# Optimization experiments

Measured on AMD Instinct MI355X. Metric: run time of the kernel, lower is better.

Reference implementation:

```python
import jax, jax.numpy as jnp
import numpy as np

# dims (see shape_source)
B, N, P, H, M, E, HOPS = 512, 102, 12, 256, 4, 3, 2
C_CLIP = 10.0   # logit clipping constant params['C']
T = 1.0         # temperature params['T']
NEG = -1e9


def setup_inputs() -> dict:
    key = jax.random.key(0)
    ks = jax.random.split(key, 18)
    s = 0.08  # uniform init range as in _initialize_weights, use scaled normals
    inp = {
        "node_features": jax.random.normal(ks[0], (B, N, P), jnp.float32),
        "adjacency": jax.random.uniform(ks[1], (B, E, N, N), jnp.float32),  # per-edge-cat weighted adjacency
        "mask": jax.random.randint(ks[2], (B, N), 0, 2).astype(jnp.int32),  # 1 = already scheduled / forbidden
        # encoder params
        "W_emb": jax.random.normal(ks[3], (P, H), jnp.float32) * s,
        "W_rel": jax.random.normal(ks[4], (HOPS, E, H, H), jnp.float32) * s / np.sqrt(H),
        "W_self": jax.random.normal(ks[5], (HOPS, H, H), jnp.float32) * s / np.sqrt(H),
        # multi-head glimpse params (Vec / W_q / W_ref per head)
        "Vec": jax.random.normal(ks[6], (M, H, H), jnp.float32) * s,
        "W_q": jax.random.normal(ks[7], (M, 3 * H, H), jnp.float32) * s,
        "W_ref": jax.random.normal(ks[8], (M, H, H), jnp.float32) * s,
        "W_mh": jax.random.normal(ks[9], (M * H, H), jnp.float32) * s,  # multi_head_embedding
        # final pointer params
        "Vec2": jax.random.normal(ks[10], (H,), jnp.float32) * s,
        "W_q2": jax.random.normal(ks[11], (H, H), jnp.float32) * s,
        "W_ref2": jax.random.normal(ks[12], (H, H), jnp.float32) * s,
        # learned decoder seed vectors
        "dec_input": jax.random.normal(ks[13], (H,), jnp.float32) * s,
        "v_1": jax.random.normal(ks[14], (H,), jnp.float32) * s,
    }
    return inp


def reference(node_features, adjacency, mask, W_emb, W_rel, W_self, Vec, W_q,
              W_ref, W_mh, Vec2, W_q2, W_ref2, dec_input, v_1):
    # ---- encoder: linear embedding + HOPS of relational (per-edge-category) message passing ----
    h = jnp.einsum('bnp,ph->bnh', node_features, W_emb)            # [B,N,H]
    for hop in range(HOPS):
        msg = jnp.einsum('benm,bmh->benh', adjacency, h)           # gather neighbors per edge cat
        h = jax.nn.relu(jnp.einsum('benh,ehk->bnk', msg, W_rel[hop])
                        + jnp.einsum('bnh,hk->bnk', h, W_self[hop]))
    enc = h                                                         # [B,N,H]

    # ---- decoder query: cat(graph readout, learned dec_input, learned v_1) -> 3H ----
    enc_mean = enc.mean(axis=1)                                     # [B,H]
    q_cat = jnp.concatenate([enc_mean,
                             jnp.broadcast_to(dec_input, (B, H)),
                             jnp.broadcast_to(v_1, (B, H))], axis=-1)  # [B,3H]

    # ---- multi-head additive (Bahdanau) glimpse: per-head Vec/W_q/W_ref tanh scoring ----
    q = jnp.einsum('bf,mfh->bmh', q_cat, W_q)                       # [B,M,H]
    r = jnp.einsum('bnh,mhk->bmnk', enc, W_ref)                     # [B,M,N,H]
    u = jnp.einsum('bmnh,mhk->bmnk', jnp.tanh(q[:, :, None, :] + r), Vec)
    scores = u.sum(axis=-1)                                         # [B,M,N]
    scores = jnp.where(mask[:, None, :] > 0, NEG, scores)
    a = jax.nn.softmax(scores, axis=-1)
    ctx = jnp.einsum('bmn,bnh->bmh', a, enc).reshape(B, M * H)
    query2 = ctx @ W_mh                                             # [B,H]

    # ---- final pointer head (Vec2 / W_q2 / W_ref2) ----
    u2 = jnp.einsum('h,bnh->bn', Vec2,
                    jnp.tanh((query2 @ W_q2)[:, None, :] + jnp.einsum('bnh,hk->bnk', enc, W_ref2)))
    u2 = C_CLIP * jnp.tanh(u2)                                      # logit clipping
    u2 = jnp.where(mask > 0, NEG, u2)
    log_p = jax.nn.log_softmax(u2 / T, axis=-1)                     # [B,N]
    return log_p
```

## Files before the change

### kernel.cpp

```cpp
#include <hip/hip_runtime.h>
#include <hip/hip_bf16.h>

#define B 512
#define N 102
#define Pdim 12
#define H 256
#define M 4
#define E 3
#define NEG (-1e9f)
#define RT 52224
#define NN 10404

typedef __hip_bfloat16 bf16;
typedef __attribute__((ext_vector_type(8))) short short8;
typedef __attribute__((ext_vector_type(4))) float f32x4;
typedef __attribute__((ext_vector_type(16))) float f32x16;

__device__ __forceinline__ float b2f(bf16 v) { return __bfloat162float(v); }
__device__ __forceinline__ bf16 f2b(float v) { return __float2bfloat16(v); }
__device__ __forceinline__ short f2bs(float v) {
    bf16 t = __float2bfloat16(v);
    return *reinterpret_cast<short*>(&t);
}
__device__ __forceinline__ float fast_tanh(float x) {
    float e = __expf(2.f * x);
    return 1.f - 2.f * __builtin_amdgcn_rcpf(e + 1.f);
}

__global__ __launch_bounds__(256) void wt_prep(const float* __restrict__ Wrel,
                                               const float* __restrict__ Wself,
                                               const float* __restrict__ Wref,
                                               const float* __restrict__ Wref2,
                                               const float* __restrict__ Wmh,
                                               const float* __restrict__ Wq2,
                                               const float* __restrict__ W_q,
                                               const float* __restrict__ Vec,
                                               const float* __restrict__ W_emb,
                                               const float* __restrict__ dec,
                                               const float* __restrict__ v1,
                                               const float* __restrict__ adj,
                                               short* __restrict__ wfrag,
                                               short* __restrict__ wrefT,
                                               short* __restrict__ wref2T,
                                               short* __restrict__ wmh_bf,
                                               short* __restrict__ wq2_bf,
                                               short* __restrict__ wq_bf,
                                               short* __restrict__ wembf,
                                               short* __restrict__ adjp,
                                               float* __restrict__ qconst,
                                               float* __restrict__ vsum) {
    int bid = blockIdx.x;
    int tid = threadIdx.x;
    __shared__ short tl[1024 * 17];
    if (bid >= 3652) {
        int be = bid - 3652;
        const float* src = adj + (size_t)be * NN;
        short* dst = adjp + (size_t)be * (112 * 128);
        for (int i = tid; i < 112 * 128; i += 256) {
            int n = i >> 7, m = i & 127;
            short v = 0;
            if (n < N && m < N) v = f2bs(src[n * N + m]);
            dst[i] = v;
        }
        return;
    }
    if (bid < 32) {
        int hop = bid >> 4, ct = bid & 15;
        for (int i = tid; i < 16384; i += 256) {
            int k = i >> 4, c0 = i & 15;
            int c = ct * 16 + c0;
            float v;
            if (k < 768) v = Wrel[(((size_t)hop * E + (k >> 8)) * H + (k & 255)) * H + c];
            else         v = Wself[((size_t)hop * H + (k - 768)) * H + c];
            tl[k * 17 + c0] = f2bs(v);
        }
        __syncthreads();
        short8* outp = (short8*)wfrag + (size_t)(hop * 16 + ct) * 2048;
        for (int i = tid; i < 2048; i += 256) {
            int ks = i >> 6, lq = i & 63;
            int c0 = lq & 15, kb = (lq >> 4) * 8;
            short8 v;
#pragma unroll
            for (int j = 0; j < 8; ++j) v[j] = tl[(ks * 32 + kb + j) * 17 + c0];
            outp[i] = v;
        }
        return;
    }
    if (bid >= 3648) {
        int m = bid - 3648, hh = tid;
        __shared__ float dls[H], vls[H];
        dls[hh] = dec[hh];
        vls[hh] = v1[hh];
        __syncthreads();
        const float* Wm = W_q + (size_t)m * (3 * H) * H;
        float s = 0.f;
        for (int f = 0; f < H; ++f)
            s += dls[f] * Wm[(H + f) * H + hh] + vls[f] * Wm[(2 * H + f) * H + hh];
        qconst[m * H + hh] = s;
        float vs = 0.f;
        const float* Vr = Vec + ((size_t)m * H + hh) * H;
        for (int k = 0; k < H; ++k) vs += Vr[k];
        vsum[m * H + hh] = vs;
        return;
    }
    int idx = 524288 + (bid - 32) * 256 + tid;
    if (idx < 786432) {
        int r = idx - 524288;
        int row = r >> 8, k = r & 255;
        int m = row >> 8, c = row & 255;
        wrefT[r] = f2bs(Wref[((size_t)m * H + k) * H + c]);
    } else if (idx < 851968) {
        int r = idx - 786432;
        int c = r >> 8, k = r & 255;
        wref2T[r] = f2bs(Wref2[k * H + c]);
    } else if (idx < 1114112) {
        int r = idx - 851968;
        wmh_bf[r] = f2bs(Wmh[r]);
    } else if (idx < 1179648) {
        int r = idx - 1114112;
        wq2_bf[r] = f2bs(Wq2[r]);
    } else if (idx < 1441792) {
        int r = idx - 1179648;
        int m = r >> 16, fh = r & 65535;
        wq_bf[r] = f2bs(W_q[(size_t)m * 768 * 256 + fh]);
    } else if (idx < 1449984) {
        int r = idx - 1441792;
        int ct = r >> 9, lq = (r >> 3) & 63, j = r & 7;
        int c = ct * 16 + (lq & 15), k = (lq >> 4) * 8 + j;
        wembf[r] = (k < Pdim) ? f2bs(W_emb[k * H + c]) : (short)0;
    }
}

#define HP 264
#define YP2 136
#define ASP 136
__global__ __launch_bounds__(512, 2) void enc_fused(const float* __restrict__ nf,
                                                    const short* __restrict__ wembf,
                                                    const short* __restrict__ adjp,
                                                    const short* __restrict__ wfragp,
                                                    bf16* __restrict__ enc_out,
                                                    float* __restrict__ mean_out) {
    int b = blockIdx.x;
    int tid = threadIdx.x;
    int w = tid >> 6;
    int l = tid & 63;
    int cg = l & 15;
    int rg = l >> 4;
    int ct0 = 2 * w, ct1 = ct0 + 1;

    __shared__ short hS[112 * HP];
    __shared__ short YtS[256 * YP2];
    __shared__ short AsS[112 * ASP];

    const short8 z8 = {0, 0, 0, 0, 0, 0, 0, 0};
    for (int i = tid; i < 10 * 32; i += 512) {
        int n = 102 + (i >> 5), g = i & 31;
        *(short8*)(&hS[n * HP + g * 8]) = z8;
    }
    {
        int c = tid >> 1, g = 14 + (tid & 1);
        *(short8*)(&YtS[c * YP2 + g * 8]) = z8;
    }

    {
        const short8* we8 = (const short8*)wembf;
        short8 bfe0 = we8[ct0 * 64 + l];
        short8 bfe1 = we8[ct1 * 64 + l];
#pragma unroll
        for (int nt = 0; nt < 7; ++nt) {
            int row = nt * 16 + cg;
            short8 afr = z8;
            if (row < 102 && rg < 2) {
                const float* src = nf + ((size_t)b * N + row) * Pdim + rg * 8;
                f32x4 v0 = *(const f32x4*)src;
                afr[0] = f2bs(v0[0]); afr[1] = f2bs(v0[1]);
                afr[2] = f2bs(v0[2]); afr[3] = f2bs(v0[3]);
                if (rg == 0) {
                    f32x4 v1 = *(const f32x4*)(src + 4);
                    afr[4] = f2bs(v1[0]); afr[5] = f2bs(v1[1]);
                    afr[6] = f2bs(v1[2]); afr[7] = f2bs(v1[3]);
                }
            }
            f32x4 d0 = (f32x4){0.f, 0.f, 0.f, 0.f}, d1 = d0;
            d0 = __builtin_amdgcn_mfma_f32_16x16x32_bf16(afr, bfe0, d0, 0, 0, 0);
            d1 = __builtin_amdgcn_mfma_f32_16x16x32_bf16(afr, bfe1, d1, 0, 0, 0);
#pragma unroll
            for (int r = 0; r < 4; ++r) {
                int n = nt * 16 + rg * 4 + r;
                hS[n * HP + ct0 * 16 + cg] = f2bs(d0[r]);
                hS[n * HP + ct1 * 16 + cg] = f2bs(d1[r]);
            }
        }
    }
    __syncthreads();

    for (int hop = 0; hop < 2; ++hop) {
        const short8* wf8 = ((const short8*)wfragp) + (size_t)hop * 32768;
        f32x4 hacc0[7], hacc1[7];
#pragma unroll
        for (int j = 0; j < 7; ++j) {
            hacc0[j] = (f32x4){0.f, 0.f, 0.f, 0.f};
            hacc1[j] = hacc0[j];
        }

        for (int e = 0; e < E; ++e) {
            const short8* Ap = (const short8*)adjp + (size_t)(b * E + e) * 1792;
            for (int i = tid; i < 1792; i += 512) {
                int n = i >> 4, g = i & 15;
                *(short8*)(&AsS[n * ASP + g * 8]) = Ap[i];
            }
            if (e == 0) {
#pragma unroll
                for (int ks = 0; ks < 8; ++ks) {
                    short8 wfs0 = wf8[(ct0 * 32 + 24 + ks) * 64 + l];
                    short8 wfs1 = wf8[(ct1 * 32 + 24 + ks) * 64 + l];
#pragma unroll
                    for (int nt = 0; nt < 7; ++nt) {
                        short8 hf = *(const short8*)(&hS[(nt * 16 + cg) * HP + ks * 32 + rg * 8]);
                        hacc0[nt] = __builtin_amdgcn_mfma_f32_16x16x32_bf16(hf, wfs0, hacc0[nt], 0, 0, 0);
                        hacc1[nt] = __builtin_amdgcn_mfma_f32_16x16x32_bf16(hf, wfs1, hacc1[nt], 0, 0, 0);
                    }
                }
            }
            f32x4 g0[7], g1[7];
#pragma unroll
            for (int j = 0; j < 7; ++j) {
                g0[j] = (f32x4){0.f, 0.f, 0.f, 0.f};
                g1[j] = g0[j];
            }
#pragma unroll
            for (int ks = 0; ks < 8; ++ks) {
                short8 wfa0 = wf8[(ct0 * 32 + e * 8 + ks) * 64 + l];
                short8 wfa1 = wf8[(ct1 * 32 + e * 8 + ks) * 64 + l];
#pragma unroll
                for (int mt = 0; mt < 7; ++mt) {
                    short8 hf = *(const short8*)(&hS[(mt * 16 + cg) * HP + ks * 32 + rg * 8]);
                    g0[mt] = __builtin_amdgcn_mfma_f32_16x16x32_bf16(wfa0, hf, g0[mt], 0, 0, 0);
                    g1[mt] = __builtin_amdgcn_mfma_f32_16x16x32_bf16(wfa1, hf, g1[mt], 0, 0, 0);
                }
            }
#pragma unroll
            for (int mt = 0; mt < 7; ++mt)
#pragma unroll
                for (int r = 0; r < 4; ++r) {
                    int c0 = ct0 * 16 + rg * 4 + r;
                    int c1 = ct1 * 16 + rg * 4 + r;
                    YtS[c0 * YP2 + mt * 16 + cg] = f2bs(g0[mt][r]);
                    YtS[c1 * YP2 + mt * 16 + cg] = f2bs(g1[mt][r]);
                }
            __syncthreads();
#pragma unroll
            for (int ks = 0; ks < 4; ++ks) {
                short8 yf0 = *(const short8*)(&YtS[(ct0 * 16 + cg) * YP2 + (ks * 4 + rg) * 8]);
                short8 yf1 = *(const short8*)(&YtS[(ct1 * 16 + cg) * YP2 + (ks * 4 + rg) * 8]);
#pragma unroll
                for (int nt = 0; nt < 7; ++nt) {
                    short8 af = *(const short8*)(&AsS[(nt * 16 + cg) * ASP + ks * 32 + rg * 8]);
                    hacc0[nt] = __builtin_amdgcn_mfma_f32_16x16x32_bf16(af, yf0, hacc0[nt], 0, 0, 0);
                    hacc1[nt] = __builtin_amdgcn_mfma_f32_16x16x32_bf16(af, yf1, hacc1[nt], 0, 0, 0);
                }
            }
            __syncthreads();
        }
#pragma unroll
        for (int nt = 0; nt < 7; ++nt)
#pragma unroll
            for (int r = 0; r < 4; ++r) {
                int n = nt * 16 + rg * 4 + r;
                float v0 = hacc0[nt][r], v1 = hacc1[nt][r];
                hS[n * HP + ct0 * 16 + cg] = f2bs(v0 > 0.f ? v0 : 0.f);
                hS[n * HP + ct1 * 16 + cg] = f2bs(v1 > 0.f ? v1 : 0.f);
            }
        __syncthreads();
    }

    short* ho = (short*)enc_out;
    for (int i = tid; i < 102 * 32; i += 512) {
        int n = i >> 5, g = i & 31;
        *(short8*)(ho + ((size_t)b * N + n) * H + g * 8) = *(const short8*)(&hS[n * HP + g * 8]);
    }
    {
        float* partf = (float*)AsS;
        int c = tid & 255, qq = tid >> 8;
        float s = 0.f;
        for (int n = qq; n < N; n += 2) s += b2f(*(const bf16*)&hS[n * HP + c]);
        partf[qq * 256 + c] = s;
        __syncthreads();
        if (tid < 256)
            mean_out[(size_t)b * H + tid] = (partf[tid] + partf[256 + tid]) * (1.f / (float)N);
    }
}

__global__ __launch_bounds__(256, 2) void head2_mfma(const bf16* __restrict__ X,
                                                     const short* __restrict__ WT,
                                                     const float* __restrict__ qb, int qbs,
                                                     const float* __restrict__ vsb,
                                                     float* __restrict__ outp, int obs) {
    int rt = blockIdx.x, m = blockIdx.y;
    int r0 = rt * 128;
    int tid = threadIdx.x;
    int w = tid >> 6, l = tid & 63;
    int lr = l & 31;
    int lh = l >> 5;
    __shared__ short Xs[128 * 256];
    __shared__ float qls[3 * 256];
    __shared__ float part[4][128];

    const short* Xp = (const short*)X;
#pragma unroll
    for (int i = 0; i < 16; ++i) {
        int id = tid + i * 256;
        int r = id >> 5, g = id & 31;
        short8 v = *(const short8*)(Xp + (size_t)(r0 + r) * H + g * 8);
        *(short8*)((char*)Xs + r * 512 + ((g ^ (r & 7)) * 16)) = v;
    }
    int b_base = r0 / N;
#pragma unroll
    for (int i = 0; i < 3; ++i) {
        int bb = b_base + i;
        if (bb > B - 1) bb = B - 1;
        qls[i * 256 + tid] = qb[(size_t)bb * qbs + m * H + tid];
    }
    const short8* w8 = (const short8*)WT;
    int cbase = m * 256 + w * 64;
    short8 afr0[16], afr1[16];
#pragma unroll
    for (int ks = 0; ks < 16; ++ks) {
        afr0[ks] = w8[(size_t)(cbase + lr) * 32 + ks * 2 + lh];
        afr1[ks] = w8[(size_t)(cbase + 32 + lr) * 32 + ks * 2 + lh];
    }
    float vsl[32];
#pragma unroll
    for (int j = 0; j < 16; ++j) {
        int cl = (j & 3) + 8 * (j >> 2) + 4 * lh;
        vsl[j]      = vsb[m * H + w * 64 + cl];
        vsl[16 + j] = vsb[m * H + w * 64 + 32 + cl];
    }
    __syncthreads();

    int swz = lr & 7;
    for (int t = 0; t < 4; ++t) {
        f32x16 acc0, acc1;
#pragma unroll
        for (int j = 0; j < 16; ++j) { acc0[j] = 0.f; acc1[j] = 0.f; }
        const char* xbase = (const char*)Xs + (t * 32 + lr) * 512;
#pragma unroll
        for (int ks = 0; ks < 16; ++ks) {
            short8 bx = *(const short8*)(xbase + (((2 * ks + lh) ^ swz) * 16));
            acc0 = __builtin_amdgcn_mfma_f32_32x32x16_bf16(afr0[ks], bx, acc0, 0, 0, 0);
            acc1 = __builtin_amdgcn_mfma_f32_32x32x16_bf16(afr1[ks], bx, acc1, 0, 0, 0);
        }
        int r = r0 + t * 32 + lr;
        int b = r / N;
        int boff = b - b_base;
        float s = 0.f;
#pragma unroll
        for (int j = 0; j < 16; ++j) {
            int cl = (j & 3) + 8 * (j >> 2) + 4 * lh;
            float x0 = qls[boff * 256 + w * 64 + cl] + acc0[j];
            s += fast_tanh(x0) * vsl[j];
            float x1 = qls[boff * 256 + w * 64 + 32 + cl] + acc1[j];
            s += fast_tanh(x1) * vsl[16 + j];
        }
        s += __shfl_xor(s, 32, 64);
        if (l < 32) part[w][t * 32 + lr] = s;
    }
    __syncthreads();
    if (tid < 128) {
        int r = r0 + tid;
        int b = r / N, n = r - b * N;
        outp[(size_t)b * obs + m * N + n] = part[0][tid] + part[1][tid] + part[2][tid] + part[3][tid];
    }
}

__global__ __launch_bounds__(256) void q_k(const float* __restrict__ enc_mean,
                                           const short* __restrict__ wq_bf,
                                           const float* __restrict__ qconst,
                                           float* __restrict__ qbuf) {
    int bid = blockIdx.x;
    int b = bid >> 2, m = bid & 3;
    int hh = threadIdx.x;
    __shared__ float em[H];
    em[hh] = enc_mean[(size_t)b * H + hh];
    __syncthreads();
    const bf16* Wm = (const bf16*)(wq_bf + (size_t)m * 65536);
    float s = qconst[m * H + hh];
    for (int f = 0; f < H; ++f) s += em[f] * b2f(Wm[f * H + hh]);
    qbuf[((size_t)b * M + m) * H + hh] = s;
}

__global__ __launch_bounds__(256) void softmax_ctx_k(const float* __restrict__ scores,
                                                     const int* __restrict__ mask,
                                                     const bf16* __restrict__ enc,
                                                     float* __restrict__ ctx) {
    int bid = blockIdx.x;
    int b = bid >> 2, m = bid & 3;
    int tid = threadIdx.x;
    __shared__ float a[128];
    __shared__ float red[2];
    float sv = NEG;
    if (tid < N)
        sv = (mask[(size_t)b * N + tid] > 0) ? NEG : scores[((size_t)b * M + m) * N + tid];
    if (tid < 128) a[tid] = sv;
    __syncthreads();
    if (tid < 64) {
        float v = fmaxf(a[tid], a[tid + 64]);
        v = fmaxf(v, __shfl_xor(v, 32, 64));
        v = fmaxf(v, __shfl_xor(v, 16, 64));
        v = fmaxf(v, __shfl_xor(v, 8, 64));
        v = fmaxf(v, __shfl_xor(v, 4, 64));
        v = fmaxf(v, __shfl_xor(v, 2, 64));
        v = fmaxf(v, __shfl_xor(v, 1, 64));
        if (tid == 0) red[0] = v;
    }
    __syncthreads();
    float mx = red[0];
    float ev = (tid < N) ? __expf(sv - mx) : 0.f;
    if (tid < 128) a[tid] = ev;
    __syncthreads();
    if (tid < 64) {
        float v = a[tid] + a[tid + 64];
        v += __shfl_xor(v, 32, 64);
        v += __shfl_xor(v, 16, 64);
        v += __shfl_xor(v, 8, 64);
        v += __shfl_xor(v, 4, 64);
        v += __shfl_xor(v, 2, 64);
        v += __shfl_xor(v, 1, 64);
        if (tid == 0) red[1] = __builtin_amdgcn_rcpf(v);
    }
    __syncthreads();
    float inv = red[1];
    float c = 0.f;
    for (int n = 0; n < N; ++n)
        c += a[n] * b2f(enc[((size_t)b * N + n) * H + tid]);
    ctx[((size_t)b * M + m) * H + tid] = c * inv;
}

__global__ __launch_bounds__(256) void query2_k(const float* __restrict__ ctx,
                                                const short* __restrict__ wmh,
                                                const short* __restrict__ wq2,
                                                float* __restrict__ q2) {
    int b = blockIdx.x;
    int tid = threadIdx.x;
    __shared__ float cx[M * H];
    __shared__ float qy[H];
    for (int idx = tid; idx < M * H; idx += 256) cx[idx] = ctx[(size_t)b * M * H + idx];
    __syncthreads();
    const bf16* wm = (const bf16*)wmh;
    float acc = 0.f;
    for (int j = 0; j < M * H; ++j) acc += cx[j] * b2f(wm[(size_t)j * H + tid]);
    qy[tid] = acc;
    __syncthreads();
    const bf16* w2 = (const bf16*)wq2;
    float acc2 = 0.f;
    for (int k = 0; k < H; ++k) acc2 += qy[k] * b2f(w2[(size_t)k * H + tid]);
    q2[(size_t)b * H + tid] = acc2;
}

__global__ __launch_bounds__(128) void final_out_k(const float* __restrict__ u2,
                                                   const int* __restrict__ mask,
                                                   float* __restrict__ out) {
    int b = blockIdx.x;
    int tid = threadIdx.x;
    __shared__ float a[128];
    __shared__ float red[2];
    float u = NEG;
    if (tid < N) {
        u = 10.f * fast_tanh(u2[(size_t)b * N + tid]);
        if (mask[(size_t)b * N + tid] > 0) u = NEG;
    }
    a[tid] = u;
    __syncthreads();
    if (tid < 64) {
        float v = fmaxf(a[tid], a[tid + 64]);
        v = fmaxf(v, __shfl_xor(v, 32, 64));
        v = fmaxf(v, __shfl_xor(v, 16, 64));
        v = fmaxf(v, __shfl_xor(v, 8, 64));
        v = fmaxf(v, __shfl_xor(v, 4, 64));
        v = fmaxf(v, __shfl_xor(v, 2, 64));
        v = fmaxf(v, __shfl_xor(v, 1, 64));
        if (tid == 0) red[0] = v;
    }
    __syncthreads();
    float mx = red[0];
    float ev = (tid < N) ? __expf(u - mx) : 0.f;
    a[tid] = ev;
    __syncthreads();
    if (tid < 64) {
        float v = a[tid] + a[tid + 64];
        v += __shfl_xor(v, 32, 64);
        v += __shfl_xor(v, 16, 64);
        v += __shfl_xor(v, 8, 64);
        v += __shfl_xor(v, 4, 64);
        v += __shfl_xor(v, 2, 64);
        v += __shfl_xor(v, 1, 64);
        if (tid == 0) red[1] = logf(v);
    }
    __syncthreads();
    if (tid < N) out[(size_t)b * N + tid] = (u - mx) - red[1];
}

extern "C" void kernel_launch(void* const* d_in, const int* in_sizes, int n_in,
                              void* d_out, int out_size, void* d_ws, size_t ws_size,
                              hipStream_t stream) {
    const float* nf     = (const float*)d_in[0];
    const float* adj    = (const float*)d_in[1];
    const int*   mask   = (const int*)d_in[2];
    const float* W_emb  = (const float*)d_in[3];
    const float* W_rel  = (const float*)d_in[4];
    const float* W_self = (const float*)d_in[5];
    const float* Vec    = (const float*)d_in[6];
    const float* W_q    = (const float*)d_in[7];
    const float* W_ref  = (const float*)d_in[8];
    const float* W_mh   = (const float*)d_in[9];
    const float* Vec2   = (const float*)d_in[10];
    const float* W_q2   = (const float*)d_in[11];
    const float* W_ref2 = (const float*)d_in[12];
    const float* dec    = (const float*)d_in[13];
    const float* v_1    = (const float*)d_in[14];
    float* out = (float*)d_out;

    char* p = (char*)d_ws;
    size_t off = 0;
    auto alloc = [&](size_t bytes) -> char* {
        char* q = p + off;
        off += (bytes + 255) & ~(size_t)255;
        return q;
    };
    bf16* hA      = (bf16*)alloc((size_t)RT * H * sizeof(bf16));
    short* adjp   = (short*)alloc((size_t)B * E * 112 * 128 * sizeof(short));
    short* wfrag  = (short*)alloc(524288 * sizeof(short));
    short* wrefT  = (short*)alloc(262144 * sizeof(short));
    short* wref2T = (short*)alloc(65536 * sizeof(short));
    short* wmh_bf = (short*)alloc(262144 * sizeof(short));
    short* wq2_bf = (short*)alloc(65536 * sizeof(short));
    short* wq_bf  = (short*)alloc(262144 * sizeof(short));
    short* wembf  = (short*)alloc(8192 * sizeof(short));
    float* enc_mean = (float*)alloc((size_t)B * H * sizeof(float));
    float* qconst   = (float*)alloc((size_t)M * H * sizeof(float));
    float* vsumb    = (float*)alloc((size_t)M * H * sizeof(float));
    float* qbuf     = (float*)alloc((size_t)B * M * H * sizeof(float));
    float* scoresb  = (float*)alloc((size_t)B * M * N * sizeof(float));
    float* ctxb     = (float*)alloc((size_t)B * M * H * sizeof(float));
    float* q2b      = (float*)alloc((size_t)B * H * sizeof(float));
    float* u2b      = (float*)alloc((size_t)B * N * sizeof(float));

    wt_prep<<<5188, 256, 0, stream>>>(W_rel, W_self, W_ref, W_ref2, W_mh, W_q2,
                                      W_q, Vec, W_emb, dec, v_1, adj,
                                      wfrag, wrefT, wref2T, wmh_bf, wq2_bf, wq_bf, wembf,
                                      adjp, qconst, vsumb);

    enc_fused<<<B, 512, 0, stream>>>(nf, wembf, adjp, wfrag, hA, enc_mean);

    const bf16* enc = hA;

    q_k<<<B * M, 256, 0, stream>>>(enc_mean, wq_bf, qconst, qbuf);
    head2_mfma<<<dim3(RT / 128, M), 256, 0, stream>>>(enc, wrefT, qbuf, M * H, vsumb, scoresb, M * N);
    softmax_ctx_k<<<B * M, 256, 0, stream>>>(scoresb, mask, enc, ctxb);
    query2_k<<<B, 256, 0, stream>>>(ctxb, wmh_bf, wq2_bf, q2b);
    head2_mfma<<<dim3(RT / 128, 1), 256, 0, stream>>>(enc, wref2T, q2b, H, Vec2, u2b, N);
    final_out_k<<<B, 128, 0, stream>>>(u2b, mask, out);
}
```

Measured before the change: 270.1 us.

## Fuse adjacency conversion into encoder, widen encoder blocks, loop heads inside scoring kernel

The separate pass that converted and padded the adjacency tensor to bf16 is removed. The encoder now reads fp32 adjacency directly and converts it into shared memory, saving a full global write and re-read of the padded copy. The encoder block grows from 512 to 1024 threads, with each half of the waves taking a subset of the row tiles. The multi-head scoring kernel now loops over all heads inside one block, so the enc tile is loaded into shared memory once instead of once per head. The risks are a scalar, uncoalesced fp32 adjacency load with integer division, and fewer blocks for the head kernel.

```diff
diff --git a/kernel.cpp b/kernel.cpp
--- a/kernel.cpp
+++ b/kernel.cpp
@@ -38,7 +38,6 @@
                                                const float* __restrict__ W_emb,
                                                const float* __restrict__ dec,
                                                const float* __restrict__ v1,
-                                               const float* __restrict__ adj,
                                                short* __restrict__ wfrag,
                                                short* __restrict__ wrefT,
                                                short* __restrict__ wref2T,
@@ -46,24 +45,11 @@
                                                short* __restrict__ wq2_bf,
                                                short* __restrict__ wq_bf,
                                                short* __restrict__ wembf,
-                                               short* __restrict__ adjp,
                                                float* __restrict__ qconst,
                                                float* __restrict__ vsum) {
     int bid = blockIdx.x;
     int tid = threadIdx.x;
     __shared__ short tl[1024 * 17];
-    if (bid >= 3652) {
-        int be = bid - 3652;
-        const float* src = adj + (size_t)be * NN;
-        short* dst = adjp + (size_t)be * (112 * 128);
-        for (int i = tid; i < 112 * 128; i += 256) {
-            int n = i >> 7, m = i & 127;
-            short v = 0;
-            if (n < N && m < N) v = f2bs(src[n * N + m]);
-            dst[i] = v;
-        }
-        return;
-    }
     if (bid < 32) {
         int hop = bid >> 4, ct = bid & 15;
         for (int i = tid; i < 16384; i += 256) {
@@ -134,32 +120,43 @@
 #define HP 264
 #define YP2 136
 #define ASP 136
-__global__ __launch_bounds__(512, 2) void enc_fused(const float* __restrict__ nf,
-                                                    const short* __restrict__ wembf,
-                                                    const short* __restrict__ adjp,
-                                                    const short* __restrict__ wfragp,
-                                                    bf16* __restrict__ enc_out,
-                                                    float* __restrict__ mean_out) {
+__global__ __launch_bounds__(1024, 4) void enc_fused(const float* __restrict__ nf,
+                                                     const short* __restrict__ wembf,
+                                                     const float* __restrict__ adj,
+                                                     const short* __restrict__ wfragp,
+                                                     bf16* __restrict__ enc_out,
+                                                     float* __restrict__ mean_out) {
     int b = blockIdx.x;
     int tid = threadIdx.x;
     int w = tid >> 6;
     int l = tid & 63;
     int cg = l & 15;
     int rg = l >> 4;
-    int ct0 = 2 * w, ct1 = ct0 + 1;
+    int cgrp = w & 7;
+    int half = w >> 3;
+    int ct0 = 2 * cgrp, ct1 = ct0 + 1;
+    int t0 = half * 4;
 
     __shared__ short hS[112 * HP];
     __shared__ short YtS[256 * YP2];
     __shared__ short AsS[112 * ASP];
 
     const short8 z8 = {0, 0, 0, 0, 0, 0, 0, 0};
-    for (int i = tid; i < 10 * 32; i += 512) {
+    for (int i = tid; i < 10 * 32; i += 1024) {
         int n = 102 + (i >> 5), g = i & 31;
         *(short8*)(&hS[n * HP + g * 8]) = z8;
     }
-    {
+    if (tid < 512) {
         int c = tid >> 1, g = 14 + (tid & 1);
         *(short8*)(&YtS[c * YP2 + g * 8]) = z8;
+    }
+    for (int i = tid; i < 160; i += 1024) {
+        int n = 102 + (i >> 4), g = i & 15;
+        *(short8*)(&AsS[n * ASP + g * 8]) = z8;
+    }
+    for (int i = tid; i < 102 * 26; i += 1024) {
+        int n = i / 26, m = 102 + (i % 26);
+        AsS[n * ASP + m] = 0;
     }
 
     {
@@ -167,28 +164,31 @@
         short8 bfe0 = we8[ct0 * 64 + l];
         short8 bfe1 = we8[ct1 * 64 + l];
 #pragma unroll
-        for (int nt = 0; nt < 7; ++nt) {
-            int row = nt * 16 + cg;
-            short8 afr = z8;
-            if (row < 102 && rg < 2) {
-                const float* src = nf + ((size_t)b * N + row) * Pdim + rg * 8;
-                f32x4 v0 = *(const f32x4*)src;
-                afr[0] = f2bs(v0[0]); afr[1] = f2bs(v0[1]);
-                afr[2] = f2bs(v0[2]); afr[3] = f2bs(v0[3]);
-                if (rg == 0) {
-                    f32x4 v1 = *(const f32x4*)(src + 4);
-                    afr[4] = f2bs(v1[0]); afr[5] = f2bs(v1[1]);
-                    afr[6] = f2bs(v1[2]); afr[7] = f2bs(v1[3]);
-                }
-            }
-            f32x4 d0 = (f32x4){0.f, 0.f, 0.f, 0.f}, d1 = d0;
-            d0 = __builtin_amdgcn_mfma_f32_16x16x32_bf16(afr, bfe0, d0, 0, 0, 0);
-            d1 = __builtin_amdgcn_mfma_f32_16x16x32_bf16(afr, bfe1, d1, 0, 0, 0);
-#pragma unroll
-            for (int r = 0; r < 4; ++r) {
-                int n = nt * 16 + rg * 4 + r;
-                hS[n * HP + ct0 * 16 + cg] = f2bs(d0[r]);
-                hS[n * HP + ct1 * 16 + cg] = f2bs(d1[r]);
+        for (int j = 0; j < 4; ++j) {
+            if (j < 3 || half == 0) {
+                int nt = t0 + j;
+                int row = nt * 16 + cg;
+                short8 afr = z8;
+                if (row < 102 && rg < 2) {
+                    const float* src = nf + ((size_t)b * N + row) * Pdim + rg * 8;
+                    f32x4 v0 = *(const f32x4*)src;
+                    afr[0] = f2bs(v0[0]); afr[1] = f2bs(v0[1]);
+                    afr[2] = f2bs(v0[2]); afr[3] = f2bs(v0[3]);
+                    if (rg == 0) {
+                        f32x4 v1 = *(const f32x4*)(src + 4);
+                        afr[4] = f2bs(v1[0]); afr[5] = f2bs(v1[1]);
+                        afr[6] = f2bs(v1[2]); afr[7] = f2bs(v1[3]);
+                    }
+                }
+                f32x4 d0 = (f32x4){0.f, 0.f, 0.f, 0.f}, d1 = d0;
+                d0 = __builtin_amdgcn_mfma_f32_16x16x32_bf16(afr, bfe0, d0, 0, 0, 0);
+                d1 = __builtin_amdgcn_mfma_f32_16x16x32_bf16(afr, bfe1, d1, 0, 0, 0);
+#pragma unroll
+                for (int r = 0; r < 4; ++r) {
+                    int n = nt * 16 + rg * 4 + r;
+                    hS[n * HP + ct0 * 16 + cg] = f2bs(d0[r]);
+                    hS[n * HP + ct1 * 16 + cg] = f2bs(d1[r]);
+                }
             }
         }
     }
@@ -196,18 +196,18 @@
 
     for (int hop = 0; hop < 2; ++hop) {
         const short8* wf8 = ((const short8*)wfragp) + (size_t)hop * 32768;
-        f32x4 hacc0[7], hacc1[7];
-#pragma unroll
-        for (int j = 0; j < 7; ++j) {
+        f32x4 hacc0[4], hacc1[4];
+#pragma unroll
+        for (int j = 0; j < 4; ++j) {
             hacc0[j] = (f32x4){0.f, 0.f, 0.f, 0.f};
             hacc1[j] = hacc0[j];
         }
 
         for (int e = 0; e < E; ++e) {
-            const short8* Ap = (const short8*)adjp + (size_t)(b * E + e) * 1792;
-            for (int i = tid; i < 1792; i += 512) {
-                int n = i >> 4, g = i & 15;
-                *(short8*)(&AsS[n * ASP + g * 8]) = Ap[i];
+            const float* Ae = adj + ((size_t)b * E + e) * NN;
+            for (int i = tid; i < NN; i += 1024) {
+                int n = i / N, m = i - n * N;
+                AsS[n * ASP + m] = f2bs(Ae[i]);
             }
             if (e == 0) {
 #pragma unroll
@@ -215,16 +215,19 @@
                     short8 wfs0 = wf8[(ct0 * 32 + 24 + ks) * 64 + l];
                     short8 wfs1 = wf8[(ct1 * 32 + 24 + ks) * 64 + l];
 #pragma unroll
-                    for (int nt = 0; nt < 7; ++nt) {
-                        short8 hf = *(const short8*)(&hS[(nt * 16 + cg) * HP + ks * 32 + rg * 8]);
-                        hacc0[nt] = __builtin_amdgcn_mfma_f32_16x16x32_bf16(hf, wfs0, hacc0[nt], 0, 0, 0);
-                        hacc1[nt] = __builtin_amdgcn_mfma_f32_16x16x32_bf16(hf, wfs1, hacc1[nt], 0, 0, 0);
+                    for (int j = 0; j < 4; ++j) {
+                        if (j < 3 || half == 0) {
+                            int nt = t0 + j;
+                            short8 hf = *(const short8*)(&hS[(nt * 16 + cg) * HP + ks * 32 + rg * 8]);
+                            hacc0[j] = __builtin_amdgcn_mfma_f32_16x16x32_bf16(hf, wfs0, hacc0[j], 0, 0, 0);
+                            hacc1[j] = __builtin_amdgcn_mfma_f32_16x16x32_bf16(hf, wfs1, hacc1[j], 0, 0, 0);
+                        }
                     }
                 }
             }
-            f32x4 g0[7], g1[7];
-#pragma unroll
-            for (int j = 0; j < 7; ++j) {
+            f32x4 g0[4], g1[4];
+#pragma unroll
+            for (int j = 0; j < 4; ++j) {
                 g0[j] = (f32x4){0.f, 0.f, 0.f, 0.f};
                 g1[j] = g0[j];
             }
@@ -233,49 +236,61 @@
                 short8 wfa0 = wf8[(ct0 * 32 + e * 8 + ks) * 64 + l];
                 short8 wfa1 = wf8[(ct1 * 32 + e * 8 + ks) * 64 + l];
 #pragma unroll
-                for (int mt = 0; mt < 7; ++mt) {
-                    short8 hf = *(const short8*)(&hS[(mt * 16 + cg) * HP + ks * 32 + rg * 8]);
-                    g0[mt] = __builtin_amdgcn_mfma_f32_16x16x32_bf16(wfa0, hf, g0[mt], 0, 0, 0);
-                    g1[mt] = __builtin_amdgcn_mfma_f32_16x16x32_bf16(wfa1, hf, g1[mt], 0, 0, 0);
-                }
-            }
-#pragma unroll
-            for (int mt = 0; mt < 7; ++mt)
-#pragma unroll
-                for (int r = 0; r < 4; ++r) {
-                    int c0 = ct0 * 16 + rg * 4 + r;
-                    int c1 = ct1 * 16 + rg * 4 + r;
-                    YtS[c0 * YP2 + mt * 16 + cg] = f2bs(g0[mt][r]);
-                    YtS[c1 * YP2 + mt * 16 + cg] = f2bs(g1[mt][r]);
-                }
+                for (int j = 0; j < 4; ++j) {
+                    if (j < 3 || half == 0) {
+                        int mt = t0 + j;
+                        short8 hf = *(const short8*)(&hS[(mt * 16 + cg) * HP + ks * 32 + rg * 8]);
+                        g0[j] = __builtin_amdgcn_mfma_f32_16x16x32_bf16(wfa0, hf, g0[j], 0, 0, 0);
+                        g1[j] = __builtin_amdgcn_mfma_f32_16x16x32_bf16(wfa1, hf, g1[j], 0, 0, 0);
+                    }
+                }
+            }
+#pragma unroll
+            for (int j = 0; j < 4; ++j) {
+                if (j < 3 || half == 0) {
+                    int mt = t0 + j;
+#pragma unroll
+                    for (int r = 0; r < 4; ++r) {
+                        YtS[(ct0 * 16 + rg * 4 + r) * YP2 + mt * 16 + cg] = f2bs(g0[j][r]);
+                        YtS[(ct1 * 16 + rg * 4 + r) * YP2 + mt * 16 + cg] = f2bs(g1[j][r]);
+                    }
+                }
+            }
             __syncthreads();
 #pragma unroll
             for (int ks = 0; ks < 4; ++ks) {
                 short8 yf0 = *(const short8*)(&YtS[(ct0 * 16 + cg) * YP2 + (ks * 4 + rg) * 8]);
                 short8 yf1 = *(const short8*)(&YtS[(ct1 * 16 + cg) * YP2 + (ks * 4 + rg) * 8]);
 #pragma unroll
-                for (int nt = 0; nt < 7; ++nt) {
-                    short8 af = *(const short8*)(&AsS[(nt * 16 + cg) * ASP + ks * 32 + rg * 8]);
-                    hacc0[nt] = __builtin_amdgcn_mfma_f32_16x16x32_bf16(af, yf0, hacc0[nt], 0, 0, 0);
-                    hacc1[nt] = __builtin_amdgcn_mfma_f32_16x16x32_bf16(af, yf1, hacc1[nt], 0, 0, 0);
+                for (int j = 0; j < 4; ++j) {
+                    if (j < 3 || half == 0) {
+                        int nt = t0 + j;
+                        short8 af = *(const short8*)(&AsS[(nt * 16 + cg) * ASP + ks * 32 + rg * 8]);
+                        hacc0[j] = __builtin_amdgcn_mfma_f32_16x16x32_bf16(af, yf0, hacc0[j], 0, 0, 0);
+                        hacc1[j] = __builtin_amdgcn_mfma_f32_16x16x32_bf16(af, yf1, hacc1[j], 0, 0, 0);
+                    }
                 }
             }
             __syncthreads();
         }
 #pragma unroll
-        for (int nt = 0; nt < 7; ++nt)
-#pragma unroll
-            for (int r = 0; r < 4; ++r) {
-                int n = nt * 16 + rg * 4 + r;
-                float v0 = hacc0[nt][r], v1 = hacc1[nt][r];
-                hS[n * HP + ct0 * 16 + cg] = f2bs(v0 > 0.f ? v0 : 0.f);
-                hS[n * HP + ct1 * 16 + cg] = f2bs(v1 > 0.f ? v1 : 0.f);
-            }
+        for (int j = 0; j < 4; ++j) {
+            if (j < 3 || half == 0) {
+                int nt = t0 + j;
+#pragma unroll
+                for (int r = 0; r < 4; ++r) {
+                    int n = nt * 16 + rg * 4 + r;
+                    float v0 = hacc0[j][r], v1 = hacc1[j][r];
+                    hS[n * HP + ct0 * 16 + cg] = f2bs(v0 > 0.f ? v0 : 0.f);
+                    hS[n * HP + ct1 * 16 + cg] = f2bs(v1 > 0.f ? v1 : 0.f);
+                }
+            }
+        }
         __syncthreads();
     }
 
     short* ho = (short*)enc_out;
-    for (int i = tid; i < 102 * 32; i += 512) {
+    for (int i = tid; i < 102 * 32; i += 1024) {
         int n = i >> 5, g = i & 31;
         *(short8*)(ho + ((size_t)b * N + n) * H + g * 8) = *(const short8*)(&hS[n * HP + g * 8]);
     }
@@ -283,11 +298,12 @@
         float* partf = (float*)AsS;
         int c = tid & 255, qq = tid >> 8;
         float s = 0.f;
-        for (int n = qq; n < N; n += 2) s += b2f(*(const bf16*)&hS[n * HP + c]);
+        for (int n = qq; n < N; n += 4) s += b2f(*(const bf16*)&hS[n * HP + c]);
         partf[qq * 256 + c] = s;
         __syncthreads();
         if (tid < 256)
-            mean_out[(size_t)b * H + tid] = (partf[tid] + partf[256 + tid]) * (1.f / (float)N);
+            mean_out[(size_t)b * H + tid] =
+                (partf[tid] + partf[256 + tid] + partf[512 + tid] + partf[768 + tid]) * (1.f / (float)N);
     }
 }
 
@@ -295,15 +311,16 @@
                                                      const short* __restrict__ WT,
                                                      const float* __restrict__ qb, int qbs,
                                                      const float* __restrict__ vsb,
-                                                     float* __restrict__ outp, int obs) {
-    int rt = blockIdx.x, m = blockIdx.y;
+                                                     float* __restrict__ outp, int obs,
+                                                     int mcnt) {
+    int rt = blockIdx.x;
     int r0 = rt * 128;
     int tid = threadIdx.x;
     int w = tid >> 6, l = tid & 63;
     int lr = l & 31;
     int lh = l >> 5;
     __shared__ short Xs[128 * 256];
-    __shared__ float qls[3 * 256];
+    __shared__ float qls[12 * 256];
     __shared__ float part[4][128];
 
     const short* Xp = (const short*)X;
@@ -315,61 +332,67 @@
         *(short8*)((char*)Xs + r * 512 + ((g ^ (r & 7)) * 16)) = v;
     }
     int b_base = r0 / N;
-#pragma unroll
-    for (int i = 0; i < 3; ++i) {
-        int bb = b_base + i;
+    for (int i = tid; i < 3 * mcnt * 256; i += 256) {
+        int boff = i / (mcnt * 256);
+        int rem = i - boff * (mcnt * 256);
+        int m = rem >> 8, c = rem & 255;
+        int bb = b_base + boff;
         if (bb > B - 1) bb = B - 1;
-        qls[i * 256 + tid] = qb[(size_t)bb * qbs + m * H + tid];
-    }
-    const short8* w8 = (const short8*)WT;
-    int cbase = m * 256 + w * 64;
-    short8 afr0[16], afr1[16];
-#pragma unroll
-    for (int ks = 0; ks < 16; ++ks) {
-        afr0[ks] = w8[(size_t)(cbase + lr) * 32 + ks * 2 + lh];
-        afr1[ks] = w8[(size_t)(cbase + 32 + lr) * 32 + ks * 2 + lh];
-    }
-    float vsl[32];
-#pragma unroll
-    for (int j = 0; j < 16; ++j) {
-        int cl = (j & 3) + 8 * (j >> 2) + 4 * lh;
-        vsl[j]      = vsb[m * H + w * 64 + cl];
-        vsl[16 + j] = vsb[m * H + w * 64 + 32 + cl];
+        qls[(boff * mcnt + m) * 256 + c] = qb[(size_t)bb * qbs + m * H + c];
     }
     __syncthreads();
 
     int swz = lr & 7;
-    for (int t = 0; t < 4; ++t) {
-        f32x16 acc0, acc1;
-#pragma unroll
-        for (int j = 0; j < 16; ++j) { acc0[j] = 0.f; acc1[j] = 0.f; }
-        const char* xbase = (const char*)Xs + (t * 32 + lr) * 512;
+    for (int m = 0; m < mcnt; ++m) {
+        const short8* w8 = (const short8*)(WT + (size_t)m * H * H);
+        int cbase = w * 64;
+        short8 afr0[16], afr1[16];
 #pragma unroll
         for (int ks = 0; ks < 16; ++ks) {
-            short8 bx = *(const short8*)(xbase + (((2 * ks + lh) ^ swz) * 16));
-            acc0 = __builtin_amdgcn_mfma_f32_32x32x16_bf16(afr0[ks], bx, acc0, 0, 0, 0);
-            acc1 = __builtin_amdgcn_mfma_f32_32x32x16_bf16(afr1[ks], bx, acc1, 0, 0, 0);
-        }
-        int r = r0 + t * 32 + lr;
-        int b = r / N;
-        int boff = b - b_base;
-        float s = 0.f;
+            afr0[ks] = w8[(size_t)(cbase + lr) * 32 + ks * 2 + lh];
+            afr1[ks] = w8[(size_t)(cbase + 32 + lr) * 32 + ks * 2 + lh];
+        }
+        float vsl[32];
 #pragma unroll
         for (int j = 0; j < 16; ++j) {
             int cl = (j & 3) + 8 * (j >> 2) + 4 * lh;
-            float x0 = qls[boff * 256 + w * 64 + cl] + acc0[j];
-            s += fast_tanh(x0) * vsl[j];
-            float x1 = qls[boff * 256 + w * 64 + 32 + cl] + acc1[j];
-            s += fast_tanh(x1) * vsl[16 + j];
-        }
-        s += __shfl_xor(s, 32, 64);
-        if (l < 32) part[w][t * 32 + lr] = s;
-    }
-    __syncthreads();
-    if (tid < 128) {
-        int r = r0 + tid;
-        int b = r / N, n = r - b * N;
-        outp[(size_t)b * obs + m * N + n] = part[0][tid] + part[1][tid] + part[2][tid] + part[3][tid];
+            vsl[j]      = vsb[m * H + w * 64 + cl];
+            vsl[16 + j] = vsb[m * H + w * 64 + 32 + cl];
+        }
+        for (int t = 0; t < 4; ++t) {
+            f32x16 acc0, acc1;
+#pragma unroll
+            for (int j = 0; j < 16; ++j) { acc0[j] = 0.f; acc1[j] = 0.f; }
+            const char* xbase = (const char*)Xs + (t * 32 + lr) * 512;
+#pragma unroll
+            for (int ks = 0; ks < 16; ++ks) {
+                short8 bx = *(const short8*)(xbase + (((2 * ks + lh) ^ swz) * 16));
+                acc0 = __builtin_amdgcn_mfma_f32_32x32x16_bf16(afr0[ks], bx, acc0, 0, 0, 0);
+                acc1 = __builtin_amdgcn_mfma_f32_32x32x16_bf16(afr1[ks], bx, acc1, 0, 0, 0);
+            }
+            int r = r0 + t * 32 + lr;
+            int b = r / N;
+            int boff = b - b_base;
+            const float* qrow = &qls[(boff * mcnt + m) * 256];
+            float s = 0.f;
+#pragma unroll
+            for (int j = 0; j < 16; ++j) {
+                int cl = (j & 3) + 8 * (j >> 2) + 4 * lh;
+                float x0 = qrow[w * 64 + cl] + acc0[j];
+                s += fast_tanh(x0) * vsl[j];
+                float x1 = qrow[w * 64 + 32 + cl] + acc1[j];
+                s += fast_tanh(x1) * vsl[16 + j];
+            }
+            s += __shfl_xor(s, 32, 64);
+            if (l < 32) part[w][t * 32 + lr] = s;
+        }
+        __syncthreads();
+        if (tid < 128) {
+            int r = r0 + tid;
+            int b = r / N, n = r - b * N;
+            outp[(size_t)b * obs + m * N + n] = part[0][tid] + part[1][tid] + part[2][tid] + part[3][tid];
+        }
+        __syncthreads();
     }
 }
 
@@ -528,7 +551,6 @@
         return q;
     };
     bf16* hA      = (bf16*)alloc((size_t)RT * H * sizeof(bf16));
-    short* adjp   = (short*)alloc((size_t)B * E * 112 * 128 * sizeof(short));
     short* wfrag  = (short*)alloc(524288 * sizeof(short));
     short* wrefT  = (short*)alloc(262144 * sizeof(short));
     short* wref2T = (short*)alloc(65536 * sizeof(short));
@@ -545,19 +567,19 @@
     float* q2b      = (float*)alloc((size_t)B * H * sizeof(float));
     float* u2b      = (float*)alloc((size_t)B * N * sizeof(float));
 
-    wt_prep<<<5188, 256, 0, stream>>>(W_rel, W_self, W_ref, W_ref2, W_mh, W_q2,
-                                      W_q, Vec, W_emb, dec, v_1, adj,
+    wt_prep<<<3652, 256, 0, stream>>>(W_rel, W_self, W_ref, W_ref2, W_mh, W_q2,
+                                      W_q, Vec, W_emb, dec, v_1,
                                       wfrag, wrefT, wref2T, wmh_bf, wq2_bf, wq_bf, wembf,
-                                      adjp, qconst, vsumb);
-
-    enc_fused<<<B, 512, 0, stream>>>(nf, wembf, adjp, wfrag, hA, enc_mean);
+                                      qconst, vsumb);
+
+    enc_fused<<<B, 1024, 0, stream>>>(nf, wembf, adj, wfrag, hA, enc_mean);
 
     const bf16* enc = hA;
 
     q_k<<<B * M, 256, 0, stream>>>(enc_mean, wq_bf, qconst, qbuf);
-    head2_mfma<<<dim3(RT / 128, M), 256, 0, stream>>>(enc, wrefT, qbuf, M * H, vsumb, scoresb, M * N);
+    head2_mfma<<<RT / 128, 256, 0, stream>>>(enc, wrefT, qbuf, M * H, vsumb, scoresb, M * N, M);
     softmax_ctx_k<<<B * M, 256, 0, stream>>>(scoresb, mask, enc, ctxb);
     query2_k<<<B, 256, 0, stream>>>(ctxb, wmh_bf, wq2_bf, q2b);
-    head2_mfma<<<dim3(RT / 128, 1), 256, 0, stream>>>(enc, wref2T, q2b, H, Vec2, u2b, N);
+    head2_mfma<<<RT / 128, 256, 0, stream>>>(enc, wref2T, q2b, H, Vec2, u2b, N, 1);
     final_out_k<<<B, 128, 0, stream>>>(u2b, mask, out);
 }
```

Measured after the change: 302.8 us. +12.1%, slower.

## Loop over heads inside head2_mfma and softmax_ctx to reuse staged enc tiles

Applied to the files above, without the earlier changes.

head2_mfma now loops over all heads within one block, so each 128-row enc tile is loaded into LDS once and reused for every head, where before it was reloaded once per head. softmax_ctx_k processes all four heads per batch in one block, staging the enc slice in LDS and accumulating four context vectors at once, where before the enc rows were read once per head. This cuts redundant global reads of enc. In exchange head2_mfma launches four times fewer blocks, which lowers parallelism, and needs larger LDS (qls grows to 12x256 floats, softmax uses about 54KB), which may limit occupancy.

```diff
diff --git a/kernel.cpp b/kernel.cpp
--- a/kernel.cpp
+++ b/kernel.cpp
@@ -295,15 +295,16 @@
                                                      const short* __restrict__ WT,
                                                      const float* __restrict__ qb, int qbs,
                                                      const float* __restrict__ vsb,
-                                                     float* __restrict__ outp, int obs) {
-    int rt = blockIdx.x, m = blockIdx.y;
+                                                     float* __restrict__ outp, int obs,
+                                                     int mcnt) {
+    int rt = blockIdx.x;
     int r0 = rt * 128;
     int tid = threadIdx.x;
     int w = tid >> 6, l = tid & 63;
     int lr = l & 31;
     int lh = l >> 5;
     __shared__ short Xs[128 * 256];
-    __shared__ float qls[3 * 256];
+    __shared__ float qls[12 * 256];
     __shared__ float part[4][128];
 
     const short* Xp = (const short*)X;
@@ -315,61 +316,67 @@
         *(short8*)((char*)Xs + r * 512 + ((g ^ (r & 7)) * 16)) = v;
     }
     int b_base = r0 / N;
-#pragma unroll
-    for (int i = 0; i < 3; ++i) {
-        int bb = b_base + i;
+    for (int i = tid; i < 3 * mcnt * 256; i += 256) {
+        int boff = i / (mcnt * 256);
+        int rem = i - boff * (mcnt * 256);
+        int m = rem >> 8, c = rem & 255;
+        int bb = b_base + boff;
         if (bb > B - 1) bb = B - 1;
-        qls[i * 256 + tid] = qb[(size_t)bb * qbs + m * H + tid];
-    }
-    const short8* w8 = (const short8*)WT;
-    int cbase = m * 256 + w * 64;
-    short8 afr0[16], afr1[16];
-#pragma unroll
-    for (int ks = 0; ks < 16; ++ks) {
-        afr0[ks] = w8[(size_t)(cbase + lr) * 32 + ks * 2 + lh];
-        afr1[ks] = w8[(size_t)(cbase + 32 + lr) * 32 + ks * 2 + lh];
-    }
-    float vsl[32];
-#pragma unroll
-    for (int j = 0; j < 16; ++j) {
-        int cl = (j & 3) + 8 * (j >> 2) + 4 * lh;
-        vsl[j]      = vsb[m * H + w * 64 + cl];
-        vsl[16 + j] = vsb[m * H + w * 64 + 32 + cl];
+        qls[(boff * mcnt + m) * 256 + c] = qb[(size_t)bb * qbs + m * H + c];
     }
     __syncthreads();
 
     int swz = lr & 7;
-    for (int t = 0; t < 4; ++t) {
-        f32x16 acc0, acc1;
-#pragma unroll
-        for (int j = 0; j < 16; ++j) { acc0[j] = 0.f; acc1[j] = 0.f; }
-        const char* xbase = (const char*)Xs + (t * 32 + lr) * 512;
+    for (int m = 0; m < mcnt; ++m) {
+        const short8* w8 = (const short8*)(WT + (size_t)m * H * H);
+        int cbase = w * 64;
+        short8 afr0[16], afr1[16];
 #pragma unroll
         for (int ks = 0; ks < 16; ++ks) {
-            short8 bx = *(const short8*)(xbase + (((2 * ks + lh) ^ swz) * 16));
-            acc0 = __builtin_amdgcn_mfma_f32_32x32x16_bf16(afr0[ks], bx, acc0, 0, 0, 0);
-            acc1 = __builtin_amdgcn_mfma_f32_32x32x16_bf16(afr1[ks], bx, acc1, 0, 0, 0);
-        }
-        int r = r0 + t * 32 + lr;
-        int b = r / N;
-        int boff = b - b_base;
-        float s = 0.f;
+            afr0[ks] = w8[(size_t)(cbase + lr) * 32 + ks * 2 + lh];
+            afr1[ks] = w8[(size_t)(cbase + 32 + lr) * 32 + ks * 2 + lh];
+        }
+        float vsl[32];
 #pragma unroll
         for (int j = 0; j < 16; ++j) {
             int cl = (j & 3) + 8 * (j >> 2) + 4 * lh;
-            float x0 = qls[boff * 256 + w * 64 + cl] + acc0[j];
-            s += fast_tanh(x0) * vsl[j];
-            float x1 = qls[boff * 256 + w * 64 + 32 + cl] + acc1[j];
-            s += fast_tanh(x1) * vsl[16 + j];
-        }
-        s += __shfl_xor(s, 32, 64);
-        if (l < 32) part[w][t * 32 + lr] = s;
-    }
-    __syncthreads();
-    if (tid < 128) {
-        int r = r0 + tid;
-        int b = r / N, n = r - b * N;
-        outp[(size_t)b * obs + m * N + n] = part[0][tid] + part[1][tid] + part[2][tid] + part[3][tid];
+            vsl[j]      = vsb[m * H + w * 64 + cl];
+            vsl[16 + j] = vsb[m * H + w * 64 + 32 + cl];
+        }
+        for (int t = 0; t < 4; ++t) {
+            f32x16 acc0, acc1;
+#pragma unroll
+            for (int j = 0; j < 16; ++j) { acc0[j] = 0.f; acc1[j] = 0.f; }
+            const char* xbase = (const char*)Xs + (t * 32 + lr) * 512;
+#pragma unroll
+            for (int ks = 0; ks < 16; ++ks) {
+                short8 bx = *(const short8*)(xbase + (((2 * ks + lh) ^ swz) * 16));
+                acc0 = __builtin_amdgcn_mfma_f32_32x32x16_bf16(afr0[ks], bx, acc0, 0, 0, 0);
+                acc1 = __builtin_amdgcn_mfma_f32_32x32x16_bf16(afr1[ks], bx, acc1, 0, 0, 0);
+            }
+            int r = r0 + t * 32 + lr;
+            int b = r / N;
+            int boff = b - b_base;
+            const float* qrow = &qls[(boff * mcnt + m) * 256];
+            float s = 0.f;
+#pragma unroll
+            for (int j = 0; j < 16; ++j) {
+                int cl = (j & 3) + 8 * (j >> 2) + 4 * lh;
+                float x0 = qrow[w * 64 + cl] + acc0[j];
+                s += fast_tanh(x0) * vsl[j];
+                float x1 = qrow[w * 64 + 32 + cl] + acc1[j];
+                s += fast_tanh(x1) * vsl[16 + j];
+            }
+            s += __shfl_xor(s, 32, 64);
+            if (l < 32) part[w][t * 32 + lr] = s;
+        }
+        __syncthreads();
+        if (tid < 128) {
+            int r = r0 + tid;
+            int b = r / N, n = r - b * N;
+            outp[(size_t)b * obs + m * N + n] = part[0][tid] + part[1][tid] + part[2][tid] + part[3][tid];
+        }
+        __syncthreads();
     }
 }
 
@@ -393,47 +400,63 @@
                                                      const int* __restrict__ mask,
                                                      const bf16* __restrict__ enc,
                                                      float* __restrict__ ctx) {
-    int bid = blockIdx.x;
-    int b = bid >> 2, m = bid & 3;
+    int b = blockIdx.x;
     int tid = threadIdx.x;
-    __shared__ float a[128];
-    __shared__ float red[2];
-    float sv = NEG;
-    if (tid < N)
-        sv = (mask[(size_t)b * N + tid] > 0) ? NEG : scores[((size_t)b * M + m) * N + tid];
-    if (tid < 128) a[tid] = sv;
-    __syncthreads();
-    if (tid < 64) {
-        float v = fmaxf(a[tid], a[tid + 64]);
+    int w = tid >> 6;
+    int l = tid & 63;
+    __shared__ short hEnc[102 * 264];
+    __shared__ float a[M][112];
+    __shared__ float red[M];
+
+    const short* ep = (const short*)enc;
+    for (int i = tid; i < 102 * 32; i += 256) {
+        int n = i >> 5, g = i & 31;
+        *(short8*)(&hEnc[n * 264 + g * 8]) = *(const short8*)(ep + ((size_t)b * N + n) * H + g * 8);
+    }
+    for (int i = tid; i < M * 112; i += 256) {
+        int m = i / 112, n = i % 112;
+        float s = NEG;
+        if (n < N) s = (mask[(size_t)b * N + n] > 0) ? NEG : scores[((size_t)b * M + m) * N + n];
+        a[m][n] = s;
+    }
+    __syncthreads();
+    {
+        float v = a[w][l];
+        float v2 = (l + 64 < 112) ? a[w][l + 64] : NEG;
+        v = fmaxf(v, v2);
         v = fmaxf(v, __shfl_xor(v, 32, 64));
         v = fmaxf(v, __shfl_xor(v, 16, 64));
         v = fmaxf(v, __shfl_xor(v, 8, 64));
         v = fmaxf(v, __shfl_xor(v, 4, 64));
         v = fmaxf(v, __shfl_xor(v, 2, 64));
         v = fmaxf(v, __shfl_xor(v, 1, 64));
-        if (tid == 0) red[0] = v;
-    }
-    __syncthreads();
-    float mx = red[0];
-    float ev = (tid < N) ? __expf(sv - mx) : 0.f;
-    if (tid < 128) a[tid] = ev;
-    __syncthreads();
-    if (tid < 64) {
-        float v = a[tid] + a[tid + 64];
-        v += __shfl_xor(v, 32, 64);
-        v += __shfl_xor(v, 16, 64);
-        v += __shfl_xor(v, 8, 64);
-        v += __shfl_xor(v, 4, 64);
-        v += __shfl_xor(v, 2, 64);
-        v += __shfl_xor(v, 1, 64);
-        if (tid == 0) red[1] = __builtin_amdgcn_rcpf(v);
-    }
-    __syncthreads();
-    float inv = red[1];
-    float c = 0.f;
-    for (int n = 0; n < N; ++n)
-        c += a[n] * b2f(enc[((size_t)b * N + n) * H + tid]);
-    ctx[((size_t)b * M + m) * H + tid] = c * inv;
+        float mx = __shfl(v, 0, 64);
+        float e0 = __expf(a[w][l] - mx);
+        float e1 = (l + 64 < 112) ? __expf(a[w][l + 64] - mx) : 0.f;
+        a[w][l] = e0;
+        if (l + 64 < 112) a[w][l + 64] = e1;
+        float sv = e0 + e1;
+        sv += __shfl_xor(sv, 32, 64);
+        sv += __shfl_xor(sv, 16, 64);
+        sv += __shfl_xor(sv, 8, 64);
+        sv += __shfl_xor(sv, 4, 64);
+        sv += __shfl_xor(sv, 2, 64);
+        sv += __shfl_xor(sv, 1, 64);
+        if (l == 0) red[w] = __builtin_amdgcn_rcpf(sv);
+    }
+    __syncthreads();
+    float c0 = 0.f, c1 = 0.f, c2 = 0.f, c3 = 0.f;
+    for (int n = 0; n < N; ++n) {
+        float e = b2f(*(const bf16*)&hEnc[n * 264 + tid]);
+        c0 += a[0][n] * e;
+        c1 += a[1][n] * e;
+        c2 += a[2][n] * e;
+        c3 += a[3][n] * e;
+    }
+    ctx[((size_t)b * M + 0) * H + tid] = c0 * red[0];
+    ctx[((size_t)b * M + 1) * H + tid] = c1 * red[1];
+    ctx[((size_t)b * M + 2) * H + tid] = c2 * red[2];
+    ctx[((size_t)b * M + 3) * H + tid] = c3 * red[3];
 }
 
 __global__ __launch_bounds__(256) void query2_k(const float* __restrict__ ctx,
@@ -555,9 +578,9 @@
     const bf16* enc = hA;
 
     q_k<<<B * M, 256, 0, stream>>>(enc_mean, wq_bf, qconst, qbuf);
-    head2_mfma<<<dim3(RT / 128, M), 256, 0, stream>>>(enc, wrefT, qbuf, M * H, vsumb, scoresb, M * N);
-    softmax_ctx_k<<<B * M, 256, 0, stream>>>(scoresb, mask, enc, ctxb);
+    head2_mfma<<<RT / 128, 256, 0, stream>>>(enc, wrefT, qbuf, M * H, vsumb, scoresb, M * N, M);
+    softmax_ctx_k<<<B, 256, 0, stream>>>(scoresb, mask, enc, ctxb);
     query2_k<<<B, 256, 0, stream>>>(ctxb, wmh_bf, wq2_bf, q2b);
-    head2_mfma<<<dim3(RT / 128, 1), 256, 0, stream>>>(enc, wref2T, q2b, H, Vec2, u2b, N);
+    head2_mfma<<<RT / 128, 256, 0, stream>>>(enc, wref2T, q2b, H, Vec2, u2b, N, 1);
     final_out_k<<<B, 128, 0, stream>>>(u2b, mask, out);
 }
```

Result: no change. 269.2 us (-0.3%).
